# Optimization experiments

Hardware: AMD Instinct MI355X
Metric: run time of the kernel (lower is better)

The kernel has to match this reference:

```python
import math
import jax, jax.numpy as jnp
import numpy as np

EPS = 1e-4
FMAX = 18  # max filtersize for scale clamped to 2.5: ceil(3*2^2.5+0.5)=18 -> kernel 37x37
KSZ = 2 * FMAX + 1


def _conv2d(x, w, b):
    # 3x3 conv, padding 1, NCHW / OIHW (cross-correlation, matches torch)
    y = jax.lax.conv_general_dilated(x, w, (1, 1), [(1, 1), (1, 1)],
                                     dimension_numbers=('NCHW', 'OIHW', 'NCHW'))
    return y + b[None, :, None, None]


def _basis_filters(scale):
    # scale: [B] -> [B,3,K,K] (g, dgdx, dgdy), masked to the per-sample support
    std = 2.0 ** scale                              # [B]
    fs = jnp.ceil(3.0 * std + 0.5)                  # per-sample filtersize
    x = jnp.arange(-FMAX, FMAX + 1, dtype=jnp.float32)          # [K]
    m = (jnp.abs(x)[None, :] <= fs[:, None]).astype(jnp.float32)  # [B,K] support mask
    e = jnp.exp(-0.5 * (x[None, :] / std[:, None]) ** 2) * m      # masked 1D gaussian [B,K]
    g = e[:, :, None] * e[:, None, :]                              # [B,K,K]
    g = g / jnp.sum(g, axis=(1, 2), keepdims=True)
    c = (-x[None, :] / (std[:, None] ** 3 * 2.0 * math.pi)) * e    # [B,K]
    dgdx = c[:, :, None] * e[:, None, :]   # varies along first spatial dim (x[0])
    dgdx = dgdx / jnp.sum(jnp.abs(dgdx), axis=(1, 2), keepdims=True)
    dgdy = e[:, :, None] * c[:, None, :]   # varies along second spatial dim (x[1])
    dgdy = dgdy / jnp.sum(jnp.abs(dgdy), axis=(1, 2), keepdims=True)
    return jnp.stack([g, dgdx, dgdy], axis=1)  # [B,3,K,K]


def setup_inputs() -> dict:
    key = jax.random.key(0)
    ks = jax.random.split(key, 7)
    B, H, W = 8, 512, 512
    batch = jax.random.uniform(ks[0], (B, 3, H, W), dtype=jnp.float32)
    gcm = jnp.array([[0.06, 0.63, 0.27], [0.3, 0.04, -0.35], [0.34, -0.6, 0.17]],
                    dtype=jnp.float32)
    w1 = jax.random.normal(ks[1], (16, 3, 3, 3), dtype=jnp.float32) * 0.1
    b1 = jax.random.normal(ks[2], (16,), dtype=jnp.float32) * 0.01
    w2 = jax.random.normal(ks[3], (16, 16, 3, 3), dtype=jnp.float32) * 0.1
    b2 = jax.random.normal(ks[4], (16,), dtype=jnp.float32) * 0.01
    w3 = jax.random.normal(ks[5], (1, 16, 3, 3), dtype=jnp.float32) * 0.1
    b3 = jax.random.normal(ks[6], (1,), dtype=jnp.float32) * 0.01
    return {"batch": batch, "gcm": gcm, "w1": w1, "b1": b1,
            "w2": w2, "b2": b2, "w3": w3, "b3": b3}


def reference(batch, gcm, w1, b1, w2, b2, w3, b3):
    B, _, H, W = batch.shape
    # ---- RGB order prior (non-differentiable, no_grad in torch) ----
    oh = lambda i: jax.nn.one_hot(i, 3, axis=1, dtype=batch.dtype)
    mx = jnp.argmax(batch, axis=1)                 # first max
    mn = jnp.argmin(batch, axis=1)
    bf = batch[:, ::-1]
    mx2 = 2 - jnp.argmax(bf, axis=1)               # last max
    mn2 = 2 - jnp.argmin(bf, axis=1)
    RGB_order = jax.lax.stop_gradient(
        0.5 * (oh(mx) + oh(mx2)) - 0.5 * (oh(mn) + oh(mn2)))  # [B,3,H,W]

    # ---- per-sample adaptive scale from small CNN ----
    h = jax.nn.silu(_conv2d(batch, w1, b1))
    h = jax.nn.silu(_conv2d(h, w2, b2))
    s = _conv2d(h, w3, b3)
    scale = jnp.clip(jnp.mean(s, axis=(1, 2, 3)), -2.5, 2.5)   # [B]

    # ---- Gaussian color model ----
    xg = jnp.einsum('ij,bjhw->bihw', gcm, batch)  # [B,3,H,W] -> (E, El, Ell)

    # ---- per-sample Gaussian basis convolution, batched via grouped conv ----
    basis = _basis_filters(scale)                                  # [B,3,K,K]
    xin = xg.reshape(1, B * 3, H, W)
    wk = jnp.broadcast_to(basis[:, None], (B, 3, 3, KSZ, KSZ)).reshape(B * 9, 1, KSZ, KSZ)
    out = jax.lax.conv_general_dilated(xin, wk, (1, 1), [(FMAX, FMAX), (FMAX, FMAX)],
                                       feature_group_count=B * 3,
                                       dimension_numbers=('NCHW', 'OIHW', 'NCHW'))
    out = out.reshape(B, 3, 3, H, W)   # [B, chan(E/El/Ell), filt(g/dx/dy), H, W]
    E = out[:, 0, 0:1]
    Ex = out[:, 0, 1:2]
    Ey = out[:, 0, 2:3]
    El = out[:, 1, 0:1]
    Ell = out[:, 2, 0:1]

    Hf = jnp.arctan(El / (Ell + EPS))
    S = jnp.log((El ** 2 + Ell ** 2) / (E ** 2 + EPS) + EPS)
    Ww = jnp.arctan((Ex / (E + EPS)) ** 2 + (Ey / (E + EPS)) ** 2)
    return jnp.concatenate([Hf, S, RGB_order, Ww], axis=1)  # [B,6,H,W]
```

## Files before the change

kernel.cpp:

```cpp
#include <hip/hip_runtime.h>
#include <hip/hip_bf16.h>

constexpr int BN = 8, HH = 512, WW = 512;
constexpr int PIX = HH * WW;
constexpr float EPSF = 1e-4f;

__device__ __forceinline__ float b2f(__hip_bfloat16 x) { return __bfloat162float(x); }
__device__ __forceinline__ __hip_bfloat16 f2b(float x) { return __float2bfloat16(x); }
__device__ __forceinline__ unsigned short bfbits(float x) {
    union { __hip_bfloat16 b; unsigned short u; } cv; cv.b = f2b(x); return cv.u;
}

typedef __attribute__((ext_vector_type(8))) short bf16x8;
typedef __attribute__((ext_vector_type(4))) float f32x4;

constexpr int OFF_TOT = 0;
constexpr int OFF_ROW0 = 128;
constexpr int OFF_ROW1 = 256;
constexpr int OFF_COL0 = 384;
constexpr int OFF_COL1 = 512;
constexpr int OFF_COR = 640;
constexpr int OFF_WR  = 2048;
constexpr int OFF_EH  = 4608;
constexpr int OFF_CH  = 5120;
constexpr size_t OFF_TPB = 65536;
constexpr size_t TP_BYTES = (size_t)4 * BN * PIX * 4;
constexpr size_t WS_NEEDED = OFF_TPB + TP_BYTES;

__global__ void prep_kernel(const float* __restrict__ w2, float* __restrict__ wsf) {
    int t = threadIdx.x;
    for (int i = t; i < 640; i += 256) wsf[i] = 0.f;
    unsigned short* ab = (unsigned short*)(wsf + OFF_WR);
    for (int idx = t; idx < 5120; idx += 256) {
        int part = idx / 2560;
        int id = idx - part * 2560;
        int ks = id >> 9, rem = id & 511, lane = rem >> 3, j = id & 7;
        int oc = lane & 15, q = lane >> 4;
        int k = q * 8 + j;
        int tap = 2 * ks + (k >> 4), ic = k & 15;
        float val = (tap <= 8) ? w2[oc * 144 + ic * 9 + tap] : 0.f;
        float hv = b2f(f2b(val));
        ab[idx] = (part == 0) ? bfbits(val) : bfbits(val - hv);
    }
}

__device__ __forceinline__ void conv1_px(const float v[27], const float* __restrict__ w1,
                                         const float* __restrict__ b1, unsigned int u[8]) {
    float o[16];
#pragma unroll
    for (int oc = 0; oc < 16; oc++) {
        float a = b1[oc];
#pragma unroll
        for (int j = 0; j < 27; j++) a += v[j] * w1[oc * 27 + j];
        o[oc] = a / (1.f + __expf(-a));
    }
#pragma unroll
    for (int k = 0; k < 8; k++)
        u[k] = (unsigned int)bfbits(o[2 * k]) | ((unsigned int)bfbits(o[2 * k + 1]) << 16);
}

__global__ __launch_bounds__(256) void conv12_kernel(const float* __restrict__ batch,
                                                     const float* __restrict__ w1,
                                                     const float* __restrict__ b1,
                                                     const unsigned short* __restrict__ abuf,
                                                     const float* __restrict__ b2v,
                                                     const float* __restrict__ gcm,
                                                     float* __restrict__ wsf,
                                                     float* __restrict__ out) {
    __shared__ uint4 h1s[18 * 66 * 2];
    __shared__ float part[4][16];

    int tx = threadIdx.x;
    int lane = tx & 63, wave = tx >> 6;
    int n = lane & 15, q = lane >> 4;
    int w0 = blockIdx.x * 64, h0 = blockIdx.y * 16, b = blockIdx.z;
    bool edge = (blockIdx.x == 0) || (blockIdx.x == 7) || (blockIdx.y == 0) || (blockIdx.y == 31);

    union { uint4 u; bf16x8 v; } cv;
    bf16x8 ah[5], al[5];
    const uint4* ab4 = (const uint4*)abuf;
#pragma unroll
    for (int ks = 0; ks < 5; ks++) {
        cv.u = ab4[ks * 64 + lane];       ah[ks] = cv.v;
        cv.u = ab4[320 + ks * 64 + lane]; al[ks] = cv.v;
    }

    const float* pb = batch + (size_t)(b * 3) * PIX;
    for (int i = tx; i < 18 * 66; i += 256) {
        int r = i / 66, c = i - r * 66;
        int gh = h0 - 1 + r, gw = w0 - 1 + c;
        unsigned int u[8];
        if (!edge) {
            const float* p0 = pb + (size_t)(gh - 1) * WW + (gw - 1);
            float v[27];
#pragma unroll
            for (int ic = 0; ic < 3; ic++)
#pragma unroll
                for (int kh = 0; kh < 3; kh++)
#pragma unroll
                    for (int kw = 0; kw < 3; kw++)
                        v[ic * 9 + kh * 3 + kw] = p0[(size_t)ic * PIX + kh * WW + kw];
            conv1_px(v, w1, b1, u);
        } else if (gh >= 0 && gh < HH && gw >= 0 && gw < WW) {
            float v[27];
#pragma unroll
            for (int ic = 0; ic < 3; ic++) {
                const float* p = pb + (size_t)ic * PIX;
#pragma unroll
                for (int kh = 0; kh < 3; kh++) {
                    int hh = gh + kh - 1;
#pragma unroll
                    for (int kw = 0; kw < 3; kw++) {
                        int ww = gw + kw - 1;
                        float x = 0.f;
                        if (hh >= 0 && hh < HH && ww >= 0 && ww < WW) x = p[hh * WW + ww];
                        v[ic * 9 + kh * 3 + kw] = x;
                    }
                }
            }
            conv1_px(v, w1, b1, u);
        } else {
#pragma unroll
            for (int k = 0; k < 8; k++) u[k] = 0u;
        }
        int swz = (c >> 2) & 1;
        int base = i * 2;
        h1s[base + swz]       = make_uint4(u[0], u[1], u[2], u[3]);
        h1s[base + (swz ^ 1)] = make_uint4(u[4], u[5], u[6], u[7]);
    }

    for (int j = tx; j < 1024; j += 256) {
        int rr = j >> 6, ccx = j & 63;
        size_t p = (size_t)(h0 + rr) * WW + (w0 + ccx);
        float v0 = pb[p], v1 = pb[(size_t)PIX + p], v2 = pb[2 * (size_t)PIX + p];
        int mx  = (v0 >= v1 && v0 >= v2) ? 0 : ((v1 >= v2) ? 1 : 2);
        int mx2 = (v2 >= v1 && v2 >= v0) ? 2 : ((v1 >= v0) ? 1 : 0);
        int mn  = (v0 <= v1 && v0 <= v2) ? 0 : ((v1 <= v2) ? 1 : 2);
        int mn2 = (v2 <= v1 && v2 <= v0) ? 2 : ((v1 <= v0) ? 1 : 0);
#pragma unroll
        for (int c = 0; c < 3; c++) {
            float r = 0.5f * ((float)(c == mx) + (float)(c == mx2))
                    - 0.5f * ((float)(c == mn) + (float)(c == mn2));
            out[(size_t)(b * 6 + 2 + c) * PIX + p] = r;
        }
    }
    __syncthreads();

    float tt[4] = {0, 0, 0, 0};
    float cs0[4] = {0, 0, 0, 0};
    float cs1[4] = {0, 0, 0, 0};
    for (int rloc = 0; rloc < 4; rloc++) {
        int row = wave * 4 + rloc;
        int grow = h0 + row;
        f32x4 acc[4] = {{0,0,0,0},{0,0,0,0},{0,0,0,0},{0,0,0,0}};
#pragma unroll
        for (int ks = 0; ks < 5; ks++) {
            int tap = 2 * ks + (q >> 1); if (tap > 8) tap = 8;
            int dh = tap / 3 - 1, dw = tap % 3 - 1;
            int half = q & 1;
            int lr = row + 1 + dh;
#pragma unroll
            for (int t = 0; t < 4; t++) {
                int c = 1 + dw + t * 16 + n;
                cv.u = h1s[(lr * 66 + c) * 2 + (half ^ ((c >> 2) & 1))];
                acc[t] = __builtin_amdgcn_mfma_f32_16x16x32_bf16(ah[ks], cv.v, acc[t], 0, 0, 0);
                acc[t] = __builtin_amdgcn_mfma_f32_16x16x32_bf16(al[ks], cv.v, acc[t], 0, 0, 0);
            }
        }
        float sv[4][4];
#pragma unroll
        for (int t = 0; t < 4; t++)
#pragma unroll
            for (int r = 0; r < 4; r++) {
                float a = acc[t][r] + b2v[q * 4 + r];
                sv[t][r] = a / (1.f + __expf(-a));
            }
#pragma unroll
        for (int r = 0; r < 4; r++) tt[r] += sv[0][r] + sv[1][r] + sv[2][r] + sv[3][r];
        if (grow == 0 || grow == HH - 1) {
            int off = (grow == 0) ? OFF_ROW0 : OFF_ROW1;
#pragma unroll
            for (int r = 0; r < 4; r++) {
                float x = sv[0][r] + sv[1][r] + sv[2][r] + sv[3][r];
#pragma unroll
                for (int d = 1; d < 16; d <<= 1) x += __shfl_xor(x, d, 64);
                if (n == 0) atomicAdd(&wsf[off + b * 16 + q * 4 + r], x);
            }
        }
        if (blockIdx.x == 0 && n == 0)
#pragma unroll
            for (int r = 0; r < 4; r++) cs0[r] += sv[0][r];
        if (blockIdx.x == 7 && n == 15)
#pragma unroll
            for (int r = 0; r < 4; r++) cs1[r] += sv[3][r];
        if ((grow == 0 || grow == HH - 1)) {
            int hi = (grow == 0) ? 0 : 1;
            if (blockIdx.x == 0 && n == 0)
#pragma unroll
                for (int r = 0; r < 4; r++)
                    wsf[OFF_COR + ((b * 2 + hi) * 2 + 0) * 16 + q * 4 + r] = sv[0][r];
            if (blockIdx.x == 7 && n == 15)
#pragma unroll
                for (int r = 0; r < 4; r++)
                    wsf[OFF_COR + ((b * 2 + hi) * 2 + 1) * 16 + q * 4 + r] = sv[3][r];
        }
    }
    if (blockIdx.x == 0 && n == 0)
#pragma unroll
        for (int r = 0; r < 4; r++) atomicAdd(&wsf[OFF_COL0 + b * 16 + q * 4 + r], cs0[r]);
    if (blockIdx.x == 7 && n == 15)
#pragma unroll
        for (int r = 0; r < 4; r++) atomicAdd(&wsf[OFF_COL1 + b * 16 + q * 4 + r], cs1[r]);
#pragma unroll
    for (int r = 0; r < 4; r++) {
        float x = tt[r];
#pragma unroll
        for (int d = 1; d < 16; d <<= 1) x += __shfl_xor(x, d, 64);
        tt[r] = x;
    }
    if (n == 0)
#pragma unroll
        for (int r = 0; r < 4; r++) part[wave][q * 4 + r] = tt[r];
    __syncthreads();
    if (tx < 16)
        atomicAdd(&wsf[OFF_TOT + b * 16 + tx],
                  part[0][tx] + part[1][tx] + part[2][tx] + part[3][tx]);
}

__global__ void filter_kernel(const float* __restrict__ w3, const float* __restrict__ b3,
                              float* __restrict__ wsf) {
    int b = blockIdx.x, t = threadIdx.x;
    __shared__ float red[160];
    float val = 0.f;
    if (t < 144) {
        int ic = t / 9, tap = t % 9, kh = tap / 3, kw = tap % 3;
        float T = wsf[OFF_TOT + b * 16 + ic];
        int hi = -1, wi = -1;
        if (kh == 0) { T -= wsf[OFF_ROW1 + b * 16 + ic]; hi = 1; }
        else if (kh == 2) { T -= wsf[OFF_ROW0 + b * 16 + ic]; hi = 0; }
        if (kw == 0) { T -= wsf[OFF_COL1 + b * 16 + ic]; wi = 1; }
        else if (kw == 2) { T -= wsf[OFF_COL0 + b * 16 + ic]; wi = 0; }
        if (hi >= 0 && wi >= 0) T += wsf[OFF_COR + ((b * 2 + hi) * 2 + wi) * 16 + ic];
        val = w3[t] * T;
    }
    red[t] = val;
    __syncthreads();
    __shared__ float sh_mean;
    if (t == 0) {
        float S = 0.f;
        for (int i = 0; i < 144; i++) S += red[i];
        sh_mean = b3[0] + S * (1.f / (float)PIX);
    }
    __syncthreads();
    float scale = fminf(2.5f, fmaxf(-2.5f, sh_mean));
    float sd = exp2f(scale);
    float fs = ceilf(3.f * sd + 0.5f);
    float e = 0.f, c = 0.f;
    if (t < 37) {
        float x = (float)(t - 18);
        if (fabsf(x) <= fs) {
            float qq = x / sd;
            e = __expf(-0.5f * qq * qq);
            c = -x / (sd * sd * sd * 6.28318530717958647692f) * e;
        }
    }
    __shared__ float sa[40], sb[40];
    if (t < 37) { sa[t] = e; sb[t] = fabsf(c); }
    __syncthreads();
    __shared__ float Se, Sc;
    if (t == 0) {
        float a = 0.f, d = 0.f;
        for (int i = 0; i < 37; i++) { a += sa[i]; d += sb[i]; }
        Se = a; Sc = d;
    }
    __syncthreads();
    if (t < 37) {
        wsf[OFF_EH + b * 37 + t] = e / Se;
        wsf[OFF_CH + b * 37 + t] = c / Sc;
    }
}

__global__ __launch_bounds__(256) void horiz_kernel(const float* __restrict__ batch,
                                                    const float* __restrict__ gcm,
                                                    const float* __restrict__ ehat,
                                                    const float* __restrict__ chat,
                                                    float* __restrict__ t) {
    __shared__ float xr[4][3][556];
    int tx = threadIdx.x;
    int h0 = blockIdx.x * 4;
    int b  = blockIdx.y;
    const float* pb = batch + (size_t)(b * 3) * PIX;
    float g0 = gcm[0], g1 = gcm[1], g2 = gcm[2];
    float g3 = gcm[3], g4 = gcm[4], g5 = gcm[5];
    float g6 = gcm[6], g7 = gcm[7], g8 = gcm[8];
    for (int i = tx; i < 4 * 548; i += 256) {
        int r = i / 548, c = i - r * 548;
        int gw = c - 18;
        float v0 = 0.f, v1 = 0.f, v2 = 0.f;
        if (gw >= 0 && gw < WW) {
            size_t p = (size_t)(h0 + r) * WW + gw;
            v0 = pb[p]; v1 = pb[(size_t)PIX + p]; v2 = pb[2 * (size_t)PIX + p];
        }
        xr[r][0][c] = g0 * v0 + g1 * v1 + g2 * v2;
        xr[r][1][c] = g3 * v0 + g4 * v1 + g5 * v2;
        xr[r][2][c] = g6 * v0 + g7 * v1 + g8 * v2;
    }
    __syncthreads();
    int r = tx >> 6, colbase = (tx & 63) * 8;
    const float* eh = ehat + b * 37; const float* ch = chat + b * 37;
    float a0[8] = {}, a1[8] = {}, a2[8] = {}, a3[8] = {};
#pragma unroll
    for (int k4 = 0; k4 < 11; k4++) {
        float4 x0 = *(const float4*)&xr[r][0][colbase + k4 * 4];
        float4 x1 = *(const float4*)&xr[r][1][colbase + k4 * 4];
        float4 x2 = *(const float4*)&xr[r][2][colbase + k4 * 4];
        const float* s0 = (const float*)&x0;
        const float* s1 = (const float*)&x1;
        const float* s2 = (const float*)&x2;
#pragma unroll
        for (int s = 0; s < 4; s++) {
            int kk = k4 * 4 + s;
#pragma unroll
            for (int i = 0; i < 8; i++) {
                int k = kk - i;
                if (k >= 0 && k < 37) {
                    float ce = eh[k], cc = ch[k];
                    a0[i] += ce * s0[s]; a1[i] += ce * s1[s];
                    a2[i] += ce * s2[s]; a3[i] += cc * s0[s];
                }
            }
        }
    }
    const size_t PL = (size_t)BN * PIX;
    size_t p = (size_t)b * PIX + (size_t)(h0 + r) * WW + colbase;
    *(float4*)&t[0 * PL + p]     = make_float4(a0[0], a0[1], a0[2], a0[3]);
    *(float4*)&t[0 * PL + p + 4] = make_float4(a0[4], a0[5], a0[6], a0[7]);
    *(float4*)&t[1 * PL + p]     = make_float4(a1[0], a1[1], a1[2], a1[3]);
    *(float4*)&t[1 * PL + p + 4] = make_float4(a1[4], a1[5], a1[6], a1[7]);
    *(float4*)&t[2 * PL + p]     = make_float4(a2[0], a2[1], a2[2], a2[3]);
    *(float4*)&t[2 * PL + p + 4] = make_float4(a2[4], a2[5], a2[6], a2[7]);
    *(float4*)&t[3 * PL + p]     = make_float4(a3[0], a3[1], a3[2], a3[3]);
    *(float4*)&t[3 * PL + p + 4] = make_float4(a3[4], a3[5], a3[6], a3[7]);
}

__global__ __launch_bounds__(256) void vert_kernel(const float* __restrict__ t,
                                                   const float* __restrict__ ehat,
                                                   const float* __restrict__ chat,
                                                   float* __restrict__ out) {
    int tx = threadIdx.x;
    int j = blockIdx.x * 64 + (tx & 63);
    int r0 = blockIdx.y * 32 + (tx >> 6) * 8;
    int b = blockIdx.z;
    const float* eh = ehat + b * 37; const float* ch = chat + b * 37;
    const size_t PL = (size_t)BN * PIX;
    const float* t0 = t + (size_t)b * PIX;
    float E[8] = {}, Ex[8] = {}, Ey[8] = {}, El[8] = {}, Ell[8] = {};
#pragma unroll
    for (int kk = 0; kk < 44; kk++) {
        int gr = r0 - 18 + kk;
        if (gr >= 0 && gr < HH) {
            size_t idx = (size_t)gr * WW + j;
            float v0 = t0[idx], v1 = t0[PL + idx], v2 = t0[2 * PL + idx], v3 = t0[3 * PL + idx];
#pragma unroll
            for (int i = 0; i < 8; i++) {
                int k = kk - i;
                if (k >= 0 && k < 37) {
                    float ce = eh[k], cc = ch[k];
                    E[i] += ce * v0; Ex[i] += cc * v0; Ey[i] += ce * v3;
                    El[i] += ce * v1; Ell[i] += ce * v2;
                }
            }
        }
    }
#pragma unroll
    for (int i = 0; i < 8; i++) {
        int h = r0 + i;
        float Hf = atanf(El[i] / (Ell[i] + EPSF));
        float S = logf((El[i] * El[i] + Ell[i] * Ell[i]) / (E[i] * E[i] + EPSF) + EPSF);
        float rx = Ex[i] / (E[i] + EPSF), ry = Ey[i] / (E[i] + EPSF);
        float Wv = atanf(rx * rx + ry * ry);
        size_t base = (size_t)(b * 6) * PIX + (size_t)h * WW + j;
        out[base] = Hf;
        out[base + PIX] = S;
        out[base + 5 * (size_t)PIX] = Wv;
    }
}

extern "C" void kernel_launch(void* const* d_in, const int* in_sizes, int n_in,
                              void* d_out, int out_size, void* d_ws, size_t ws_size,
                              hipStream_t stream) {
    const float* batch = (const float*)d_in[0];
    const float* gcm   = (const float*)d_in[1];
    const float* w1    = (const float*)d_in[2];
    const float* b1    = (const float*)d_in[3];
    const float* w2    = (const float*)d_in[4];
    const float* b2    = (const float*)d_in[5];
    const float* w3    = (const float*)d_in[6];
    const float* b3    = (const float*)d_in[7];
    float* out = (float*)d_out;

    if (ws_size < WS_NEEDED) return;

    float* wsf = (float*)d_ws;
    float* tpl = (float*)((char*)d_ws + OFF_TPB);
    float* ehat = wsf + OFF_EH;
    float* chat = wsf + OFF_CH;

    prep_kernel<<<dim3(1), dim3(256), 0, stream>>>(w2, wsf);
    conv12_kernel<<<dim3(8, 32, 8), dim3(256), 0, stream>>>(
        batch, w1, b1, (const unsigned short*)(wsf + OFF_WR), b2, gcm, wsf, out);
    filter_kernel<<<dim3(8), dim3(160), 0, stream>>>(w3, b3, wsf);
    horiz_kernel<<<dim3(128, 8), dim3(256), 0, stream>>>(batch, gcm, ehat, chat, tpl);
    vert_kernel<<<dim3(8, 16, 8), dim3(256), 0, stream>>>(tpl, ehat, chat, out);
}
```

Measured before the change: 269.6 us.

## Fuse filter, horizontal and vertical blur into one strip kernel; stage conv1 input in LDS

Filter construction plus the horizontal and vertical separable Gaussian passes are merged into one strip kernel. The horizontal pass writes into a rolling 68-row ring buffer in shared memory, and the vertical pass reads from it directly, so the 4-plane global intermediate and two kernel launches are gone. Conv12 now stages its batch tile with halo in shared memory and reuses it for both conv1 and the RGB-order computation, instead of issuing 27 global loads per pixel. The cost is that the strip kernel launches only 256 blocks, each doing long serial work with many barriers, and it recomputes a horizontal halo of 36 columns per 64-column tile. Together this may reduce parallelism and occupancy.

```diff
diff --git a/kernel.cpp b/kernel.cpp
--- a/kernel.cpp
+++ b/kernel.cpp
@@ -21,11 +21,7 @@
 constexpr int OFF_COL1 = 512;
 constexpr int OFF_COR = 640;
 constexpr int OFF_WR  = 2048;
-constexpr int OFF_EH  = 4608;
-constexpr int OFF_CH  = 5120;
-constexpr size_t OFF_TPB = 65536;
-constexpr size_t TP_BYTES = (size_t)4 * BN * PIX * 4;
-constexpr size_t WS_NEEDED = OFF_TPB + TP_BYTES;
+constexpr size_t WS_NEEDED = 65536;
 
 __global__ void prep_kernel(const float* __restrict__ w2, float* __restrict__ wsf) {
     int t = threadIdx.x;
@@ -64,9 +60,9 @@
                                                      const float* __restrict__ b1,
                                                      const unsigned short* __restrict__ abuf,
                                                      const float* __restrict__ b2v,
-                                                     const float* __restrict__ gcm,
                                                      float* __restrict__ wsf,
                                                      float* __restrict__ out) {
+    __shared__ float sbat[3][20][68];
     __shared__ uint4 h1s[18 * 66 * 2];
     __shared__ float part[4][16];
 
@@ -86,12 +82,22 @@
     }
 
     const float* pb = batch + (size_t)(b * 3) * PIX;
+    for (int i = tx; i < 4080; i += 256) {
+        int ch = i / 1360, rem = i - ch * 1360, r = rem / 68, c = rem - r * 68;
+        int gh = h0 - 2 + r, gw = w0 - 2 + c;
+        float x = 0.f;
+        if (!edge || (gh >= 0 && gh < HH && gw >= 0 && gw < WW))
+            x = pb[(size_t)ch * PIX + (size_t)gh * WW + gw];
+        sbat[ch][r][c] = x;
+    }
+    __syncthreads();
+
     for (int i = tx; i < 18 * 66; i += 256) {
         int r = i / 66, c = i - r * 66;
         int gh = h0 - 1 + r, gw = w0 - 1 + c;
         unsigned int u[8];
-        if (!edge) {
-            const float* p0 = pb + (size_t)(gh - 1) * WW + (gw - 1);
+        bool valid = !edge || (gh >= 0 && gh < HH && gw >= 0 && gw < WW);
+        if (valid) {
             float v[27];
 #pragma unroll
             for (int ic = 0; ic < 3; ic++)
@@ -99,25 +105,7 @@
                 for (int kh = 0; kh < 3; kh++)
 #pragma unroll
                     for (int kw = 0; kw < 3; kw++)
-                        v[ic * 9 + kh * 3 + kw] = p0[(size_t)ic * PIX + kh * WW + kw];
-            conv1_px(v, w1, b1, u);
-        } else if (gh >= 0 && gh < HH && gw >= 0 && gw < WW) {
-            float v[27];
-#pragma unroll
-            for (int ic = 0; ic < 3; ic++) {
-                const float* p = pb + (size_t)ic * PIX;
-#pragma unroll
-                for (int kh = 0; kh < 3; kh++) {
-                    int hh = gh + kh - 1;
-#pragma unroll
-                    for (int kw = 0; kw < 3; kw++) {
-                        int ww = gw + kw - 1;
-                        float x = 0.f;
-                        if (hh >= 0 && hh < HH && ww >= 0 && ww < WW) x = p[hh * WW + ww];
-                        v[ic * 9 + kh * 3 + kw] = x;
-                    }
-                }
-            }
+                        v[ic * 9 + kh * 3 + kw] = sbat[ic][r + kh][c + kw];
             conv1_px(v, w1, b1, u);
         } else {
 #pragma unroll
@@ -131,8 +119,10 @@
 
     for (int j = tx; j < 1024; j += 256) {
         int rr = j >> 6, ccx = j & 63;
+        float v0 = sbat[0][rr + 2][ccx + 2];
+        float v1 = sbat[1][rr + 2][ccx + 2];
+        float v2 = sbat[2][rr + 2][ccx + 2];
         size_t p = (size_t)(h0 + rr) * WW + (w0 + ccx);
-        float v0 = pb[p], v1 = pb[(size_t)PIX + p], v2 = pb[2 * (size_t)PIX + p];
         int mx  = (v0 >= v1 && v0 >= v2) ? 0 : ((v1 >= v2) ? 1 : 2);
         int mx2 = (v2 >= v1 && v2 >= v0) ? 2 : ((v1 >= v0) ? 1 : 0);
         int mn  = (v0 <= v1 && v0 <= v2) ? 0 : ((v1 <= v2) ? 1 : 2);
@@ -227,162 +217,163 @@
                   part[0][tx] + part[1][tx] + part[2][tx] + part[3][tx]);
 }
 
-__global__ void filter_kernel(const float* __restrict__ w3, const float* __restrict__ b3,
-                              float* __restrict__ wsf) {
-    int b = blockIdx.x, t = threadIdx.x;
+__global__ __launch_bounds__(256) void strip_kernel(const float* __restrict__ batch,
+                                                    const float* __restrict__ gcm,
+                                                    const float* __restrict__ w3,
+                                                    const float* __restrict__ b3,
+                                                    const float* __restrict__ wsf,
+                                                    float* __restrict__ out) {
+    __shared__ float tplb[68][4][64];
+    __shared__ float xst[16][3][104];
+    __shared__ float leh[37], lch[37];
     __shared__ float red[160];
-    float val = 0.f;
-    if (t < 144) {
-        int ic = t / 9, tap = t % 9, kh = tap / 3, kw = tap % 3;
-        float T = wsf[OFF_TOT + b * 16 + ic];
-        int hi = -1, wi = -1;
-        if (kh == 0) { T -= wsf[OFF_ROW1 + b * 16 + ic]; hi = 1; }
-        else if (kh == 2) { T -= wsf[OFF_ROW0 + b * 16 + ic]; hi = 0; }
-        if (kw == 0) { T -= wsf[OFF_COL1 + b * 16 + ic]; wi = 1; }
-        else if (kw == 2) { T -= wsf[OFF_COL0 + b * 16 + ic]; wi = 0; }
-        if (hi >= 0 && wi >= 0) T += wsf[OFF_COR + ((b * 2 + hi) * 2 + wi) * 16 + ic];
-        val = w3[t] * T;
-    }
-    red[t] = val;
-    __syncthreads();
-    __shared__ float sh_mean;
-    if (t == 0) {
-        float S = 0.f;
-        for (int i = 0; i < 144; i++) S += red[i];
-        sh_mean = b3[0] + S * (1.f / (float)PIX);
-    }
-    __syncthreads();
-    float scale = fminf(2.5f, fmaxf(-2.5f, sh_mean));
-    float sd = exp2f(scale);
-    float fs = ceilf(3.f * sd + 0.5f);
-    float e = 0.f, c = 0.f;
-    if (t < 37) {
-        float x = (float)(t - 18);
-        if (fabsf(x) <= fs) {
-            float qq = x / sd;
-            e = __expf(-0.5f * qq * qq);
-            c = -x / (sd * sd * sd * 6.28318530717958647692f) * e;
-        }
-    }
-    __shared__ float sa[40], sb[40];
-    if (t < 37) { sa[t] = e; sb[t] = fabsf(c); }
-    __syncthreads();
-    __shared__ float Se, Sc;
-    if (t == 0) {
-        float a = 0.f, d = 0.f;
-        for (int i = 0; i < 37; i++) { a += sa[i]; d += sb[i]; }
-        Se = a; Sc = d;
-    }
-    __syncthreads();
-    if (t < 37) {
-        wsf[OFF_EH + b * 37 + t] = e / Se;
-        wsf[OFF_CH + b * 37 + t] = c / Sc;
-    }
-}
-
-__global__ __launch_bounds__(256) void horiz_kernel(const float* __restrict__ batch,
-                                                    const float* __restrict__ gcm,
-                                                    const float* __restrict__ ehat,
-                                                    const float* __restrict__ chat,
-                                                    float* __restrict__ t) {
-    __shared__ float xr[4][3][556];
+    __shared__ float smean, sSe, sSc;
+
     int tx = threadIdx.x;
-    int h0 = blockIdx.x * 4;
-    int b  = blockIdx.y;
+    int c0 = blockIdx.x * 64, r0 = blockIdx.y * 128, b = blockIdx.z;
     const float* pb = batch + (size_t)(b * 3) * PIX;
+
+    {
+        float val = 0.f;
+        if (tx < 144) {
+            int ic = tx / 9, tap = tx % 9, kh = tap / 3, kw = tap % 3;
+            float T = wsf[OFF_TOT + b * 16 + ic];
+            int hi = -1, wi = -1;
+            if (kh == 0) { T -= wsf[OFF_ROW1 + b * 16 + ic]; hi = 1; }
+            else if (kh == 2) { T -= wsf[OFF_ROW0 + b * 16 + ic]; hi = 0; }
+            if (kw == 0) { T -= wsf[OFF_COL1 + b * 16 + ic]; wi = 1; }
+            else if (kw == 2) { T -= wsf[OFF_COL0 + b * 16 + ic]; wi = 0; }
+            if (hi >= 0 && wi >= 0) T += wsf[OFF_COR + ((b * 2 + hi) * 2 + wi) * 16 + ic];
+            val = w3[tx] * T;
+        }
+        if (tx < 160) red[tx] = val;
+        __syncthreads();
+        if (tx == 0) {
+            float S = 0.f;
+            for (int i = 0; i < 144; i++) S += red[i];
+            smean = b3[0] + S * (1.f / (float)PIX);
+        }
+        __syncthreads();
+        float scale = fminf(2.5f, fmaxf(-2.5f, smean));
+        float sd = exp2f(scale);
+        float fs = ceilf(3.f * sd + 0.5f);
+        float e = 0.f, c = 0.f;
+        if (tx < 37) {
+            float x = (float)(tx - 18);
+            if (fabsf(x) <= fs) {
+                float qq = x / sd;
+                e = __expf(-0.5f * qq * qq);
+                c = -x / (sd * sd * sd * 6.28318530717958647692f) * e;
+            }
+            red[tx] = e; red[40 + tx] = fabsf(c);
+        }
+        __syncthreads();
+        if (tx == 0) {
+            float a = 0.f, d = 0.f;
+            for (int i = 0; i < 37; i++) { a += red[i]; d += red[40 + i]; }
+            sSe = a; sSc = d;
+        }
+        __syncthreads();
+        if (tx < 37) { leh[tx] = e / sSe; lch[tx] = c / sSc; }
+        __syncthreads();
+    }
+
     float g0 = gcm[0], g1 = gcm[1], g2 = gcm[2];
     float g3 = gcm[3], g4 = gcm[4], g5 = gcm[5];
     float g6 = gcm[6], g7 = gcm[7], g8 = gcm[8];
-    for (int i = tx; i < 4 * 548; i += 256) {
-        int r = i / 548, c = i - r * 548;
-        int gw = c - 18;
-        float v0 = 0.f, v1 = 0.f, v2 = 0.f;
-        if (gw >= 0 && gw < WW) {
-            size_t p = (size_t)(h0 + r) * WW + gw;
-            v0 = pb[p]; v1 = pb[(size_t)PIX + p]; v2 = pb[2 * (size_t)PIX + p];
-        }
-        xr[r][0][c] = g0 * v0 + g1 * v1 + g2 * v2;
-        xr[r][1][c] = g3 * v0 + g4 * v1 + g5 * v2;
-        xr[r][2][c] = g6 * v0 + g7 * v1 + g8 * v2;
-    }
-    __syncthreads();
-    int r = tx >> 6, colbase = (tx & 63) * 8;
-    const float* eh = ehat + b * 37; const float* ch = chat + b * 37;
-    float a0[8] = {}, a1[8] = {}, a2[8] = {}, a3[8] = {};
-#pragma unroll
-    for (int k4 = 0; k4 < 11; k4++) {
-        float4 x0 = *(const float4*)&xr[r][0][colbase + k4 * 4];
-        float4 x1 = *(const float4*)&xr[r][1][colbase + k4 * 4];
-        float4 x2 = *(const float4*)&xr[r][2][colbase + k4 * 4];
-        const float* s0 = (const float*)&x0;
-        const float* s1 = (const float*)&x1;
-        const float* s2 = (const float*)&x2;
-#pragma unroll
-        for (int s = 0; s < 4; s++) {
-            int kk = k4 * 4 + s;
+
+    int startRow = (r0 - 18 < 0) ? 0 : r0 - 18;
+    int lastHi = startRow - 1;
+    for (int ckn = 0; ckn < 4; ckn++) {
+        int R = r0 + ckn * 32;
+        int target = R + 49; if (target > HH - 1) target = HH - 1;
+        for (int rr = lastHi + 1; rr <= target; rr += 16) {
+            int nr = target - rr + 1; if (nr > 16) nr = 16;
+            for (int i = tx; i < nr * 100; i += 256) {
+                int lr = i / 100, c = i - lr * 100;
+                int gw = c0 - 18 + c;
+                float v0 = 0.f, v1 = 0.f, v2 = 0.f;
+                if (gw >= 0 && gw < WW) {
+                    size_t p = (size_t)(rr + lr) * WW + gw;
+                    v0 = pb[p]; v1 = pb[(size_t)PIX + p]; v2 = pb[2 * (size_t)PIX + p];
+                }
+                xst[lr][0][c] = g0 * v0 + g1 * v1 + g2 * v2;
+                xst[lr][1][c] = g3 * v0 + g4 * v1 + g5 * v2;
+                xst[lr][2][c] = g6 * v0 + g7 * v1 + g8 * v2;
+            }
+            __syncthreads();
+            int lr = tx >> 4, c4 = (tx & 15) * 4;
+            if (lr < nr) {
+                float a0[4] = {}, a1[4] = {}, a2[4] = {}, a3[4] = {};
+#pragma unroll
+                for (int k4 = 0; k4 < 10; k4++) {
+                    float4 x0 = *(const float4*)&xst[lr][0][c4 + k4 * 4];
+                    float4 x1 = *(const float4*)&xst[lr][1][c4 + k4 * 4];
+                    float4 x2 = *(const float4*)&xst[lr][2][c4 + k4 * 4];
+                    const float* s0 = (const float*)&x0;
+                    const float* s1 = (const float*)&x1;
+                    const float* s2 = (const float*)&x2;
+#pragma unroll
+                    for (int s = 0; s < 4; s++) {
+                        int kk = k4 * 4 + s;
+#pragma unroll
+                        for (int i = 0; i < 4; i++) {
+                            int k = kk - i;
+                            if (k >= 0 && k < 37) {
+                                float ce = leh[k], cc = lch[k];
+                                a0[i] += ce * s0[s]; a1[i] += ce * s1[s];
+                                a2[i] += ce * s2[s]; a3[i] += cc * s0[s];
+                            }
+                        }
+                    }
+                }
+                int slot = (rr + lr) % 68;
+                *(float4*)&tplb[slot][0][c4] = make_float4(a0[0], a0[1], a0[2], a0[3]);
+                *(float4*)&tplb[slot][1][c4] = make_float4(a1[0], a1[1], a1[2], a1[3]);
+                *(float4*)&tplb[slot][2][c4] = make_float4(a2[0], a2[1], a2[2], a2[3]);
+                *(float4*)&tplb[slot][3][c4] = make_float4(a3[0], a3[1], a3[2], a3[3]);
+            }
+            __syncthreads();
+        }
+        lastHi = target;
+
+        {
+            int g = tx >> 6, c = tx & 63;
+            int base = R + g * 8;
+            int sbase = ((base - 18) % 68 + 68) % 68;
+            float E[8] = {}, Ex[8] = {}, Ey[8] = {}, El[8] = {}, Ell[8] = {};
+#pragma unroll
+            for (int kk = 0; kk < 44; kk++) {
+                int gr = base - 18 + kk;
+                if (gr >= 0 && gr < HH) {
+                    int slot = sbase + kk; if (slot >= 68) slot -= 68;
+                    float v0 = tplb[slot][0][c], v1 = tplb[slot][1][c];
+                    float v2 = tplb[slot][2][c], v3 = tplb[slot][3][c];
+#pragma unroll
+                    for (int i = 0; i < 8; i++) {
+                        int k = kk - i;
+                        if (k >= 0 && k < 37) {
+                            float ce = leh[k], cc = lch[k];
+                            E[i] += ce * v0; Ex[i] += cc * v0; Ey[i] += ce * v3;
+                            El[i] += ce * v1; Ell[i] += ce * v2;
+                        }
+                    }
+                }
+            }
 #pragma unroll
             for (int i = 0; i < 8; i++) {
-                int k = kk - i;
-                if (k >= 0 && k < 37) {
-                    float ce = eh[k], cc = ch[k];
-                    a0[i] += ce * s0[s]; a1[i] += ce * s1[s];
-                    a2[i] += ce * s2[s]; a3[i] += cc * s0[s];
-                }
-            }
-        }
-    }
-    const size_t PL = (size_t)BN * PIX;
-    size_t p = (size_t)b * PIX + (size_t)(h0 + r) * WW + colbase;
-    *(float4*)&t[0 * PL + p]     = make_float4(a0[0], a0[1], a0[2], a0[3]);
-    *(float4*)&t[0 * PL + p + 4] = make_float4(a0[4], a0[5], a0[6], a0[7]);
-    *(float4*)&t[1 * PL + p]     = make_float4(a1[0], a1[1], a1[2], a1[3]);
-    *(float4*)&t[1 * PL + p + 4] = make_float4(a1[4], a1[5], a1[6], a1[7]);
-    *(float4*)&t[2 * PL + p]     = make_float4(a2[0], a2[1], a2[2], a2[3]);
-    *(float4*)&t[2 * PL + p + 4] = make_float4(a2[4], a2[5], a2[6], a2[7]);
-    *(float4*)&t[3 * PL + p]     = make_float4(a3[0], a3[1], a3[2], a3[3]);
-    *(float4*)&t[3 * PL + p + 4] = make_float4(a3[4], a3[5], a3[6], a3[7]);
-}
-
-__global__ __launch_bounds__(256) void vert_kernel(const float* __restrict__ t,
-                                                   const float* __restrict__ ehat,
-                                                   const float* __restrict__ chat,
-                                                   float* __restrict__ out) {
-    int tx = threadIdx.x;
-    int j = blockIdx.x * 64 + (tx & 63);
-    int r0 = blockIdx.y * 32 + (tx >> 6) * 8;
-    int b = blockIdx.z;
-    const float* eh = ehat + b * 37; const float* ch = chat + b * 37;
-    const size_t PL = (size_t)BN * PIX;
-    const float* t0 = t + (size_t)b * PIX;
-    float E[8] = {}, Ex[8] = {}, Ey[8] = {}, El[8] = {}, Ell[8] = {};
-#pragma unroll
-    for (int kk = 0; kk < 44; kk++) {
-        int gr = r0 - 18 + kk;
-        if (gr >= 0 && gr < HH) {
-            size_t idx = (size_t)gr * WW + j;
-            float v0 = t0[idx], v1 = t0[PL + idx], v2 = t0[2 * PL + idx], v3 = t0[3 * PL + idx];
-#pragma unroll
-            for (int i = 0; i < 8; i++) {
-                int k = kk - i;
-                if (k >= 0 && k < 37) {
-                    float ce = eh[k], cc = ch[k];
-                    E[i] += ce * v0; Ex[i] += cc * v0; Ey[i] += ce * v3;
-                    El[i] += ce * v1; Ell[i] += ce * v2;
-                }
-            }
-        }
-    }
-#pragma unroll
-    for (int i = 0; i < 8; i++) {
-        int h = r0 + i;
-        float Hf = atanf(El[i] / (Ell[i] + EPSF));
-        float S = logf((El[i] * El[i] + Ell[i] * Ell[i]) / (E[i] * E[i] + EPSF) + EPSF);
-        float rx = Ex[i] / (E[i] + EPSF), ry = Ey[i] / (E[i] + EPSF);
-        float Wv = atanf(rx * rx + ry * ry);
-        size_t base = (size_t)(b * 6) * PIX + (size_t)h * WW + j;
-        out[base] = Hf;
-        out[base + PIX] = S;
-        out[base + 5 * (size_t)PIX] = Wv;
+                int h = base + i;
+                float Hf = atanf(El[i] / (Ell[i] + EPSF));
+                float S = logf((El[i] * El[i] + Ell[i] * Ell[i]) / (E[i] * E[i] + EPSF) + EPSF);
+                float rx = Ex[i] / (E[i] + EPSF), ry = Ey[i] / (E[i] + EPSF);
+                float Wv = atanf(rx * rx + ry * ry);
+                size_t basep = (size_t)(b * 6) * PIX + (size_t)h * WW + (c0 + c);
+                out[basep] = Hf;
+                out[basep + PIX] = S;
+                out[basep + 5 * (size_t)PIX] = Wv;
+            }
+        }
+        __syncthreads();
     }
 }
 
@@ -400,16 +391,10 @@
     float* out = (float*)d_out;
 
     if (ws_size < WS_NEEDED) return;
-
     float* wsf = (float*)d_ws;
-    float* tpl = (float*)((char*)d_ws + OFF_TPB);
-    float* ehat = wsf + OFF_EH;
-    float* chat = wsf + OFF_CH;
 
     prep_kernel<<<dim3(1), dim3(256), 0, stream>>>(w2, wsf);
     conv12_kernel<<<dim3(8, 32, 8), dim3(256), 0, stream>>>(
-        batch, w1, b1, (const unsigned short*)(wsf + OFF_WR), b2, gcm, wsf, out);
-    filter_kernel<<<dim3(8), dim3(160), 0, stream>>>(w3, b3, wsf);
-    horiz_kernel<<<dim3(128, 8), dim3(256), 0, stream>>>(batch, gcm, ehat, chat, tpl);
-    vert_kernel<<<dim3(8, 16, 8), dim3(256), 0, stream>>>(tpl, ehat, chat, out);
-}
+        batch, w1, b1, (const unsigned short*)(wsf + OFF_WR), b2, wsf, out);
+    strip_kernel<<<dim3(8, 4, 8), dim3(256), 0, stream>>>(batch, gcm, w3, b3, wsf, out);
+}
```

After: 334.0 us. 1.24x slower.
